# Kernel tuning notes

Hardware: AMD Instinct MI355X
Metric: run time of the kernel (lower is better)

## Reference

```python
import jax, jax.numpy as jnp
import numpy as np

N_NODES = 100000
N_EDGES = 3200000
IN_DIM = 64
HID_DIM = 128
OUT_DIM = 2


def setup_inputs() -> dict:
    key = jax.random.key(0)
    k1, k2, k3, k4, k5, k6 = jax.random.split(key, 6)
    x = jax.random.normal(k1, (N_NODES, IN_DIM), dtype=jnp.float32)
    edge_index = jax.random.randint(k2, (2, N_EDGES), 0, N_NODES, dtype=jnp.int64)
    W_gcn = jax.random.normal(k3, (IN_DIM, HID_DIM), dtype=jnp.float32) / np.sqrt(IN_DIM)
    b_gcn = jax.random.normal(k4, (HID_DIM,), dtype=jnp.float32) * 0.02
    W_lin = jax.random.normal(k5, (HID_DIM, OUT_DIM), dtype=jnp.float32) / np.sqrt(HID_DIM)
    b_lin = jax.random.normal(k6, (OUT_DIM,), dtype=jnp.float32) * 0.02
    return {"x": x, "edge_index": edge_index, "W_gcn": W_gcn, "b_gcn": b_gcn,
            "W_lin": W_lin, "b_lin": b_lin}


def reference(x, edge_index, W_gcn, b_gcn, W_lin, b_lin):
    # GCNConv (PyG semantics): add self-loops, symmetric deg^{-1/2} norm,
    # aggregate source->target, then relu, dropout(eval=identity), linear.
    N = x.shape[0]
    loop = jnp.arange(N, dtype=edge_index.dtype)
    src = jnp.concatenate([edge_index[0], loop])  # message sources
    dst = jnp.concatenate([edge_index[1], loop])  # message targets

    h = x @ W_gcn  # [N, HID] - transform before propagate (GCNConv order)

    ones = jnp.ones(dst.shape, dtype=h.dtype)
    deg = jax.ops.segment_sum(ones, dst, num_segments=N)  # in-degree incl. self-loop
    dinv = jnp.where(deg > 0, jax.lax.rsqrt(deg), 0.0)
    norm = dinv[src] * dinv[dst]  # [E+N]

    msg = h[src] * norm[:, None]                      # irregular gather
    agg = jax.ops.segment_sum(msg, dst, num_segments=N)  # irregular scatter-add
    agg = agg + b_gcn

    # relu -> dropout(p=0.5, eval mode => identity) -> linear head
    return jax.nn.relu(agg) @ W_lin + b_lin  # [N, OUT_DIM]
```

## Files before the change

kernel.cpp:

```cpp
#include <hip/hip_runtime.h>
#include <hip/hip_fp16.h>

#define N_NODES 100000
#define N_EDGES 3200000
#define IN_DIM 64
#define HID_DIM 128

#define RNODES 128
#define NRANGE 782
#define PCHUNK 256
#define PCHSZ (N_EDGES / PCHUNK)
#define TCAP 48
#define NLCAP 4608

#define TILE(c, r) ((size_t)(c) * NRANGE + (r))

__global__ __launch_bounds__(1024) void part_kernel(const int* __restrict__ src,
                                                    const int* __restrict__ dst,
                                                    int* __restrict__ tmp,
                                                    int* __restrict__ tcnt) {
    __shared__ int cur[NRANGE];
    const int c = blockIdx.x, tid = threadIdx.x;
    for (int i = tid; i < NRANGE; i += 1024) cur[i] = 0;
    __syncthreads();
    const int e0 = c * PCHSZ;
    int* tmpc = tmp + TILE(c, 0) * TCAP;
    int i = tid;
    for (; i + 3072 < PCHSZ; i += 4096) {
        const int dA = dst[e0 + i];
        const int sA = src[e0 + i];
        const int dB = dst[e0 + i + 1024];
        const int sB = src[e0 + i + 1024];
        const int dC = dst[e0 + i + 2048];
        const int sC = src[e0 + i + 2048];
        const int dD = dst[e0 + i + 3072];
        const int sD = src[e0 + i + 3072];
        const int rA = dA >> 7;
        const int pA = atomicAdd(&cur[rA], 1);
        if (pA < TCAP) tmpc[(size_t)rA * TCAP + pA] = sA | ((dA & 127) << 17);
        const int rB = dB >> 7;
        const int pB = atomicAdd(&cur[rB], 1);
        if (pB < TCAP) tmpc[(size_t)rB * TCAP + pB] = sB | ((dB & 127) << 17);
        const int rC = dC >> 7;
        const int pC = atomicAdd(&cur[rC], 1);
        if (pC < TCAP) tmpc[(size_t)rC * TCAP + pC] = sC | ((dC & 127) << 17);
        const int rD = dD >> 7;
        const int pD = atomicAdd(&cur[rD], 1);
        if (pD < TCAP) tmpc[(size_t)rD * TCAP + pD] = sD | ((dD & 127) << 17);
    }
    for (; i < PCHSZ; i += 1024) {
        const int d = dst[e0 + i];
        const int s = src[e0 + i];
        const int r = d >> 7;
        const int pos = atomicAdd(&cur[r], 1);
        if (pos < TCAP) tmpc[(size_t)r * TCAP + pos] = s | ((d & 127) << 17);
    }
    __syncthreads();
    for (int j = tid; j < NRANGE; j += 1024)
        tcnt[c * NRANGE + j] = min(cur[j], TCAP);
}

__global__ __launch_bounds__(512) void degscale_kernel(const int* __restrict__ tmp,
                                                       const int* __restrict__ tcnt,
                                                       const float* __restrict__ x,
                                                       int* __restrict__ degn,
                                                       float* __restrict__ dinv,
                                                       __half* __restrict__ y) {
    __shared__ int   cnt[RNODES];
    __shared__ float dvs[RNODES];
    const int r = blockIdx.x, tid = threadIdx.x;
    if (tid < RNODES) cnt[tid] = 0;
    __syncthreads();
    {
        const int c = tid >> 1, h = tid & 1;
        const int n = tcnt[c * NRANGE + r];
        const uint4* t4 = (const uint4*)(tmp + TILE(c, r) * TCAP);
        const int nv4 = (n + 3) >> 2;
        for (int v = h; v < nv4; v += 2) {
            const uint4 e = t4[v];
            const int base = v * 4;
            if (base + 0 < n) atomicAdd(&cnt[e.x >> 17], 1);
            if (base + 1 < n) atomicAdd(&cnt[e.y >> 17], 1);
            if (base + 2 < n) atomicAdd(&cnt[e.z >> 17], 1);
            if (base + 3 < n) atomicAdd(&cnt[e.w >> 17], 1);
        }
    }
    __syncthreads();
    if (tid < RNODES) {
        const int node = r * RNODES + tid;
        const int dg = cnt[tid];
        degn[node] = dg;
        const float dv = rsqrtf((float)dg + 1.0f);
        dvs[tid] = dv;
        if (node < N_NODES) dinv[node] = dv;
    }
    __syncthreads();
    for (int i = tid; i < RNODES * 16; i += 512) {
        const int nl = i >> 4, q = i & 15;
        const int node = r * RNODES + nl;
        if (node < N_NODES) {
            const float4 v = ((const float4*)x)[(size_t)node * 16 + q];
            const float dv = dvs[nl];
            __half2 h0 = __floats2half2_rn(v.x * dv, v.y * dv);
            __half2 h1 = __floats2half2_rn(v.z * dv, v.w * dv);
            uint2 pk;
            pk.x = *(unsigned int*)&h0;
            pk.y = *(unsigned int*)&h1;
            ((uint2*)y)[(size_t)node * 16 + q] = pk;
        }
    }
}

__global__ __launch_bounds__(1024) void aggb_kernel(const int* __restrict__ tmp,
                                                    const int* __restrict__ tcnt,
                                                    const int* __restrict__ degn,
                                                    const __half* __restrict__ y,
                                                    __half* __restrict__ agg) {
    __shared__ int nodelist[NLCAP];
    __shared__ int sc[RNODES];
    __shared__ int start[RNODES];
    __shared__ int cur[RNODES];
    const int r = blockIdx.x, tid = threadIdx.x;

    int mydeg = 0;
    if (tid < RNODES) {
        mydeg = degn[r * RNODES + tid];
        sc[tid] = mydeg;
    }
    __syncthreads();
    #pragma unroll
    for (int off = 1; off < RNODES; off <<= 1) {
        int v = 0;
        if (tid < RNODES && tid >= off) v = sc[tid - off];
        __syncthreads();
        if (tid < RNODES) sc[tid] += v;
        __syncthreads();
    }
    if (tid < RNODES) {
        start[tid] = sc[tid] - mydeg;
        cur[tid]   = sc[tid] - mydeg;
    }
    __syncthreads();

    {
        const int c = tid & 255, ph = tid >> 8;
        const int n = tcnt[c * NRANGE + r];
        const uint4* t4 = (const uint4*)(tmp + TILE(c, r) * TCAP);
        const int nv4 = (n + 3) >> 2;
        for (int v = ph; v < nv4; v += 4) {
            const uint4 e = t4[v];
            const int base = v * 4;
            if (base + 0 < n) {
                const int slot = atomicAdd(&cur[e.x >> 17], 1);
                if (slot < NLCAP) nodelist[slot] = e.x & 0x1FFFF;
            }
            if (base + 1 < n) {
                const int slot = atomicAdd(&cur[e.y >> 17], 1);
                if (slot < NLCAP) nodelist[slot] = e.y & 0x1FFFF;
            }
            if (base + 2 < n) {
                const int slot = atomicAdd(&cur[e.z >> 17], 1);
                if (slot < NLCAP) nodelist[slot] = e.z & 0x1FFFF;
            }
            if (base + 3 < n) {
                const int slot = atomicAdd(&cur[e.w >> 17], 1);
                if (slot < NLCAP) nodelist[slot] = e.w & 0x1FFFF;
            }
        }
    }
    __syncthreads();

    const int g = tid >> 3, lane = tid & 7;
    const uint4* y16 = (const uint4*)y;
    const int node = r * RNODES + g;
    if (node < N_NODES) {
        float accf[8];
        {
            const uint4 pk = y16[(size_t)node * 8 + lane];
            const __half2* h = (const __half2*)&pk;
            #pragma unroll
            for (int q = 0; q < 4; ++q) {
                const float2 f = __half22float2(h[q]);
                accf[2*q] = f.x; accf[2*q+1] = f.y;
            }
        }
        const int beg = start[g], end = sc[g];
        int j = beg;
        for (; j + 4 <= end; j += 4) {
            const int s0 = nodelist[j];
            const int s1 = nodelist[j + 1];
            const int s2 = nodelist[j + 2];
            const int s3 = nodelist[j + 3];
            const uint4 p0 = y16[(size_t)s0 * 8 + lane];
            const uint4 p1 = y16[(size_t)s1 * 8 + lane];
            const uint4 p2 = y16[(size_t)s2 * 8 + lane];
            const uint4 p3 = y16[(size_t)s3 * 8 + lane];
            const __half2* h0 = (const __half2*)&p0;
            const __half2* h1 = (const __half2*)&p1;
            const __half2* h2 = (const __half2*)&p2;
            const __half2* h3 = (const __half2*)&p3;
            #pragma unroll
            for (int q = 0; q < 4; ++q) {
                float2 f0 = __half22float2(h0[q]);
                float2 f1 = __half22float2(h1[q]);
                float2 f2 = __half22float2(h2[q]);
                float2 f3 = __half22float2(h3[q]);
                accf[2*q]   += (f0.x + f1.x) + (f2.x + f3.x);
                accf[2*q+1] += (f0.y + f1.y) + (f2.y + f3.y);
            }
        }
        for (; j < end; ++j) {
            const int s = nodelist[j];
            const uint4 pk = y16[(size_t)s * 8 + lane];
            const __half2* h = (const __half2*)&pk;
            #pragma unroll
            for (int q = 0; q < 4; ++q) {
                const float2 f = __half22float2(h[q]);
                accf[2*q] += f.x; accf[2*q+1] += f.y;
            }
        }
        uint4 o;
        __half2* oh = (__half2*)&o;
        #pragma unroll
        for (int q = 0; q < 4; ++q)
            oh[q] = __floats2half2_rn(accf[2*q], accf[2*q+1]);
        ((uint4*)agg)[(size_t)node * 8 + lane] = o;
    }
}

#define H_NPB 32
__global__ __launch_bounds__(256) void head_kernel(const __half* __restrict__ agg,
                                                   const float* __restrict__ dinv,
                                                   const float* __restrict__ W,
                                                   const float* __restrict__ b_gcn,
                                                   const float* __restrict__ W_lin,
                                                   const float* __restrict__ b_lin,
                                                   float* __restrict__ out) {
    __shared__ float4 Ws[IN_DIM * HID_DIM / 4];
    __shared__ float  as[H_NPB * IN_DIM];
    const int tid = threadIdx.x;

    const float4* W4 = (const float4*)W;
    #pragma unroll
    for (int i = tid; i < IN_DIM * HID_DIM / 4; i += 256) Ws[i] = W4[i];

    const int node0 = blockIdx.x * H_NPB;
    {
        const uint4 a4 = ((const uint4*)(agg + (size_t)node0 * IN_DIM))[tid];
        const __half2* h = (const __half2*)&a4;
        #pragma unroll
        for (int q = 0; q < 4; ++q) {
            const float2 f = __half22float2(h[q]);
            as[tid * 8 + 2*q]     = f.x;
            as[tid * 8 + 2*q + 1] = f.y;
        }
    }
    __syncthreads();

    const int jq = tid & 31;
    const int ng = tid >> 5;
    const float* arow = as + ng * 4 * IN_DIM;

    float4 a0 = {0,0,0,0}, a1 = {0,0,0,0}, a2 = {0,0,0,0}, a3 = {0,0,0,0};
    for (int k = 0; k < IN_DIM; ++k) {
        const float4 wv = Ws[k * 32 + jq];
        const float v0 = arow[k];
        const float v1 = arow[IN_DIM + k];
        const float v2 = arow[2 * IN_DIM + k];
        const float v3 = arow[3 * IN_DIM + k];
        a0.x += v0*wv.x; a0.y += v0*wv.y; a0.z += v0*wv.z; a0.w += v0*wv.w;
        a1.x += v1*wv.x; a1.y += v1*wv.y; a1.z += v1*wv.z; a1.w += v1*wv.w;
        a2.x += v2*wv.x; a2.y += v2*wv.y; a2.z += v2*wv.z; a2.w += v2*wv.w;
        a3.x += v3*wv.x; a3.y += v3*wv.y; a3.z += v3*wv.z; a3.w += v3*wv.w;
    }

    const float4 bg = ((const float4*)b_gcn)[jq];
    const int c0 = jq * 4;
    const float w00 = W_lin[(c0+0)*2], w01 = W_lin[(c0+0)*2+1];
    const float w10 = W_lin[(c0+1)*2], w11 = W_lin[(c0+1)*2+1];
    const float w20 = W_lin[(c0+2)*2], w21 = W_lin[(c0+2)*2+1];
    const float w30 = W_lin[(c0+3)*2], w31 = W_lin[(c0+3)*2+1];
    const float bl0 = b_lin[0], bl1 = b_lin[1];

    float4 am[4] = {a0, a1, a2, a3};
    #pragma unroll
    for (int m = 0; m < 4; ++m) {
        const int node = node0 + ng * 4 + m;
        const float dv = dinv[node];
        float4 v;
        v.x = fmaxf(am[m].x * dv + bg.x, 0.f);
        v.y = fmaxf(am[m].y * dv + bg.y, 0.f);
        v.z = fmaxf(am[m].z * dv + bg.z, 0.f);
        v.w = fmaxf(am[m].w * dv + bg.w, 0.f);
        float o0 = v.x*w00 + v.y*w10 + v.z*w20 + v.w*w30;
        float o1 = v.x*w01 + v.y*w11 + v.z*w21 + v.w*w31;
        #pragma unroll
        for (int off = 16; off > 0; off >>= 1) {
            o0 += __shfl_down(o0, off, 32);
            o1 += __shfl_down(o1, off, 32);
        }
        if (jq == 0) {
            out[(size_t)node * 2 + 0] = o0 + bl0;
            out[(size_t)node * 2 + 1] = o1 + bl1;
        }
    }
}

extern "C" void kernel_launch(void* const* d_in, const int* in_sizes, int n_in,
                              void* d_out, int out_size, void* d_ws, size_t ws_size,
                              hipStream_t stream) {
    const float* x     = (const float*)d_in[0];
    const int*   ei    = (const int*)  d_in[1];
    const float* W_gcn = (const float*)d_in[2];
    const float* b_gcn = (const float*)d_in[3];
    const float* W_lin = (const float*)d_in[4];
    const float* b_lin = (const float*)d_in[5];
    float* out = (float*)d_out;

    int*    tmp  = (int*)d_ws;
    int*    tcnt = tmp + (size_t)NRANGE * PCHUNK * TCAP;
    int*    degn = tcnt + NRANGE * PCHUNK;
    float*  dinv = (float*)(degn + NRANGE * RNODES);
    __half* y    = (__half*)(dinv + N_NODES);
    __half* agg  = y + (size_t)N_NODES * IN_DIM;

    const int* src = ei;
    const int* dst = ei + N_EDGES;

    part_kernel<<<PCHUNK, 1024, 0, stream>>>(src, dst, tmp, tcnt);
    degscale_kernel<<<NRANGE, 512, 0, stream>>>(tmp, tcnt, x, degn, dinv, y);
    aggb_kernel<<<NRANGE, 1024, 0, stream>>>(tmp, tcnt, degn, y, agg);
    head_kernel<<<N_NODES / H_NPB, 256, 0, stream>>>(agg, dinv, W_gcn, b_gcn, W_lin, b_lin, out);
}
```

Measured before the change: 210.7 us.

## Bucket each destination's neighbor list by source band for gather locality

The degree counting and nodelist bucketing now key on (destination, source band) using 8 bands derived from the upper source bits, giving 1024 sub-buckets per range. Per-node degrees become sums over bands, and the prefix scan is widened to 1024 entries. The effect is that each node's neighbor list is ordered by source region, so gathers into y fall in nearby memory and should get better cache reuse. In exchange the scan has more steps and shared-memory atomics land on more counters.

```diff
diff --git a/kernel.cpp b/kernel.cpp
--- a/kernel.cpp
+++ b/kernel.cpp
@@ -12,6 +12,7 @@
 #define PCHSZ (N_EDGES / PCHUNK)
 #define TCAP 48
 #define NLCAP 4608
+#define NBANDS 8
 
 #define TILE(c, r) ((size_t)(c) * NRANGE + (r))
 
@@ -63,13 +64,14 @@
 __global__ __launch_bounds__(512) void degscale_kernel(const int* __restrict__ tmp,
                                                        const int* __restrict__ tcnt,
                                                        const float* __restrict__ x,
-                                                       int* __restrict__ degn,
+                                                       int* __restrict__ bcnt,
                                                        float* __restrict__ dinv,
                                                        __half* __restrict__ y) {
-    __shared__ int   cnt[RNODES];
+    __shared__ int   cnt2[RNODES * NBANDS];
     __shared__ float dvs[RNODES];
     const int r = blockIdx.x, tid = threadIdx.x;
-    if (tid < RNODES) cnt[tid] = 0;
+    cnt2[tid] = 0;
+    cnt2[tid + 512] = 0;
     __syncthreads();
     {
         const int c = tid >> 1, h = tid & 1;
@@ -79,19 +81,22 @@
         for (int v = h; v < nv4; v += 2) {
             const uint4 e = t4[v];
             const int base = v * 4;
-            if (base + 0 < n) atomicAdd(&cnt[e.x >> 17], 1);
-            if (base + 1 < n) atomicAdd(&cnt[e.y >> 17], 1);
-            if (base + 2 < n) atomicAdd(&cnt[e.z >> 17], 1);
-            if (base + 3 < n) atomicAdd(&cnt[e.w >> 17], 1);
-        }
-    }
-    __syncthreads();
+            if (base + 0 < n) atomicAdd(&cnt2[(e.x >> 14) & 1023], 1);
+            if (base + 1 < n) atomicAdd(&cnt2[(e.y >> 14) & 1023], 1);
+            if (base + 2 < n) atomicAdd(&cnt2[(e.z >> 14) & 1023], 1);
+            if (base + 3 < n) atomicAdd(&cnt2[(e.w >> 14) & 1023], 1);
+        }
+    }
+    __syncthreads();
+    bcnt[r * 1024 + tid]       = cnt2[tid];
+    bcnt[r * 1024 + tid + 512] = cnt2[tid + 512];
     if (tid < RNODES) {
-        const int node = r * RNODES + tid;
-        const int dg = cnt[tid];
-        degn[node] = dg;
+        int dg = 0;
+        #pragma unroll
+        for (int b = 0; b < NBANDS; ++b) dg += cnt2[tid * NBANDS + b];
         const float dv = rsqrtf((float)dg + 1.0f);
         dvs[tid] = dv;
+        const int node = r * RNODES + tid;
         if (node < N_NODES) dinv[node] = dv;
     }
     __syncthreads();
@@ -113,33 +118,26 @@
 
 __global__ __launch_bounds__(1024) void aggb_kernel(const int* __restrict__ tmp,
                                                     const int* __restrict__ tcnt,
-                                                    const int* __restrict__ degn,
+                                                    const int* __restrict__ bcnt,
                                                     const __half* __restrict__ y,
                                                     __half* __restrict__ agg) {
     __shared__ int nodelist[NLCAP];
-    __shared__ int sc[RNODES];
-    __shared__ int start[RNODES];
-    __shared__ int cur[RNODES];
+    __shared__ int ps[RNODES * NBANDS];
+    __shared__ int cur2[RNODES * NBANDS];
     const int r = blockIdx.x, tid = threadIdx.x;
 
-    int mydeg = 0;
-    if (tid < RNODES) {
-        mydeg = degn[r * RNODES + tid];
-        sc[tid] = mydeg;
-    }
+    const int myc = bcnt[r * 1024 + tid];
+    ps[tid] = myc;
     __syncthreads();
     #pragma unroll
-    for (int off = 1; off < RNODES; off <<= 1) {
+    for (int off = 1; off < 1024; off <<= 1) {
         int v = 0;
-        if (tid < RNODES && tid >= off) v = sc[tid - off];
+        if (tid >= off) v = ps[tid - off];
         __syncthreads();
-        if (tid < RNODES) sc[tid] += v;
+        ps[tid] += v;
         __syncthreads();
     }
-    if (tid < RNODES) {
-        start[tid] = sc[tid] - mydeg;
-        cur[tid]   = sc[tid] - mydeg;
-    }
+    cur2[tid] = ps[tid] - myc;
     __syncthreads();
 
     {
@@ -151,19 +149,19 @@
             const uint4 e = t4[v];
             const int base = v * 4;
             if (base + 0 < n) {
-                const int slot = atomicAdd(&cur[e.x >> 17], 1);
+                const int slot = atomicAdd(&cur2[(e.x >> 14) & 1023], 1);
                 if (slot < NLCAP) nodelist[slot] = e.x & 0x1FFFF;
             }
             if (base + 1 < n) {
-                const int slot = atomicAdd(&cur[e.y >> 17], 1);
+                const int slot = atomicAdd(&cur2[(e.y >> 14) & 1023], 1);
                 if (slot < NLCAP) nodelist[slot] = e.y & 0x1FFFF;
             }
             if (base + 2 < n) {
-                const int slot = atomicAdd(&cur[e.z >> 17], 1);
+                const int slot = atomicAdd(&cur2[(e.z >> 14) & 1023], 1);
                 if (slot < NLCAP) nodelist[slot] = e.z & 0x1FFFF;
             }
             if (base + 3 < n) {
-                const int slot = atomicAdd(&cur[e.w >> 17], 1);
+                const int slot = atomicAdd(&cur2[(e.w >> 14) & 1023], 1);
                 if (slot < NLCAP) nodelist[slot] = e.w & 0x1FFFF;
             }
         }
@@ -184,7 +182,8 @@
                 accf[2*q] = f.x; accf[2*q+1] = f.y;
             }
         }
-        const int beg = start[g], end = sc[g];
+        const int beg = (g == 0) ? 0 : min(ps[g * NBANDS - 1], NLCAP);
+        const int end = min(ps[g * NBANDS + NBANDS - 1], NLCAP);
         int j = beg;
         for (; j + 4 <= end; j += 4) {
             const int s0 = nodelist[j];
@@ -319,8 +318,8 @@
 
     int*    tmp  = (int*)d_ws;
     int*    tcnt = tmp + (size_t)NRANGE * PCHUNK * TCAP;
-    int*    degn = tcnt + NRANGE * PCHUNK;
-    float*  dinv = (float*)(degn + NRANGE * RNODES);
+    int*    bcnt = tcnt + NRANGE * PCHUNK;
+    float*  dinv = (float*)(bcnt + NRANGE * RNODES * NBANDS);
     __half* y    = (__half*)(dinv + N_NODES);
     __half* agg  = y + (size_t)N_NODES * IN_DIM;
 
@@ -328,7 +327,7 @@
     const int* dst = ei + N_EDGES;
 
     part_kernel<<<PCHUNK, 1024, 0, stream>>>(src, dst, tmp, tcnt);
-    degscale_kernel<<<NRANGE, 512, 0, stream>>>(tmp, tcnt, x, degn, dinv, y);
-    aggb_kernel<<<NRANGE, 1024, 0, stream>>>(tmp, tcnt, degn, y, agg);
+    degscale_kernel<<<NRANGE, 512, 0, stream>>>(tmp, tcnt, x, bcnt, dinv, y);
+    aggb_kernel<<<NRANGE, 1024, 0, stream>>>(tmp, tcnt, bcnt, y, agg);
     head_kernel<<<N_NODES / H_NPB, 256, 0, stream>>>(agg, dinv, W_gcn, b_gcn, W_lin, b_lin, out);
 }
```

Measured after the change: 208.3 us. No clear change (-1.1%).
